# Kernel tuning notes

Measured on AMD Instinct MI355X. Metric: run time of the kernel, lower is better.

## Reference

```python
import jax, jax.numpy as jnp
import numpy as np

CHUNK = 128  # single steady-state chunk tier (T divisible by 128)
DECAY_MIN = 0.005


def setup_inputs() -> dict:
    key = jax.random.key(0)
    k0, k1, k2, k3, k4 = jax.random.split(key, 5)
    B, H, T, K = 4, 16, 2048, 64
    r = jax.random.normal(k0, (B, H, T, K), jnp.float32) * 0.5
    k = jax.random.normal(k1, (B, H, T, K), jnp.float32) * 0.5
    v = jax.random.normal(k2, (B, H, T, K), jnp.float32)
    # log-space decay (negative); mild magnitude keeps exp() of cumulative
    # in-chunk decays within fp32 range (torch original upcasts to fp64)
    w = -(jax.random.uniform(k3, (B, H, T, K), jnp.float32) * 0.2 + 0.01)
    u = jax.random.normal(k4, (1, H, 1, K), jnp.float32) * 0.5
    wkv_state = jnp.zeros((B, H, K, K), jnp.float32)
    return {"r": r, "k": k, "v": v, "w": w, "u": u, "wkv_state": wkv_state}


def _chunked_wkv(r, k, v, w, u, wkv_state):
    B, H, T, K = r.shape
    Tc = CHUNK
    N = T // Tc
    # decay preprocessing (log space)
    w_decay = jnp.clip(jnp.exp(w), DECAY_MIN, None)
    w_log = jnp.log(w_decay)
    wc = w_log.reshape(B, H, N, Tc, K)
    wc_cum = jnp.cumsum(wc, axis=-2)                       # inclusive cumsum
    shifted = jnp.pad(wc_cum[..., :-1, :], ((0, 0), (0, 0), (0, 0), (1, 0), (0, 0)))
    ws = wc.sum(axis=-2, keepdims=True)                    # (B,H,N,1,K)
    w_inter = jnp.exp(ws - wc_cum)                          # (B,H,N,Tc,K)
    w_intra = jnp.exp(wc_cum - wc)
    ws_e = jnp.exp(jnp.swapaxes(ws, -1, -2))               # (B,H,N,K,1)

    rc = r.reshape(B, H, N, Tc, K)
    kc = k.reshape(B, H, N, Tc, K)
    vc = v.reshape(B, H, N, Tc, K)

    # numerically-centered intra-chunk decays (offset at chunk midpoint)
    off = shifted[..., Tc // 2:Tc // 2 + 1, :]
    r_dec = jnp.exp(shifted - off)
    k_inv = jnp.exp(off - wc_cum)

    # intra-chunk attention: strictly-lower-triangular + u-bonus diagonal
    a = jnp.einsum('bhnik,bhnjk->bhnij', rc * r_dec, kc * k_inv)
    a = jnp.tril(a, -1)
    diag = jnp.einsum('bhntk,bhntk->bhnt', rc, u[:, :, None] * kc)
    a = a + diag[..., :, None] * jnp.eye(Tc, dtype=a.dtype)
    out = jnp.einsum('bhnij,bhnjv->bhniv', a, vc)

    # inter-chunk: sequential state carry via scan
    wkv = jnp.einsum('bhntk,bhntv->bhnkv', kc * w_inter, vc)   # (B,H,N,K,K)

    def step(state, inp):
        ws_i, wkv_i = inp
        return state * ws_i + wkv_i, state

    ws_s = jnp.moveaxis(ws_e, 2, 0)    # (N,B,H,K,1)
    wkv_s = jnp.moveaxis(wkv, 2, 0)    # (N,B,H,K,K)
    final_state, states = jax.lax.scan(step, wkv_state, (ws_s, wkv_s))
    states = jnp.moveaxis(states, 0, 2)  # (B,H,N,K,K) — state entering chunk n

    out = out + jnp.einsum('bhntk,bhnkv->bhntv', rc * w_intra, states)
    return out.reshape(B, H, T, K), final_state


def reference(r, k, v, w, u, wkv_state):
    return _chunked_wkv(r, k, v, w, u, wkv_state)
```

## Files before the change

kernel.cpp:

```cpp
#include <hip/hip_runtime.h>

#define TC 128
#define KD 64
#define WLOG_MIN (-5.2983174f)

typedef __attribute__((ext_vector_type(8))) short short8;
typedef __attribute__((ext_vector_type(4))) short short4_t;
typedef __attribute__((ext_vector_type(4))) float f32x4;

__device__ __forceinline__ unsigned short f2bf(float x) {
  union { float f; unsigned int u; } c; c.f = x;
  unsigned int u = c.u + 0x7fffu + ((c.u >> 16) & 1u);
  return (unsigned short)(u >> 16);
}
__device__ __forceinline__ float bf2f(unsigned short x) {
  union { unsigned int u; float f; } c; c.u = ((unsigned int)x) << 16; return c.f;
}


__global__ __launch_bounds__(512, 4)
void rwkv_intra_mfma(const float* __restrict__ rr, const float* __restrict__ kk_,
                     const float* __restrict__ vv, const float* __restrict__ ww,
                     const float* __restrict__ uu, float* __restrict__ out,
                     unsigned short* __restrict__ wkv_u16, float* __restrict__ wse_ws,
                     unsigned short* __restrict__ rw_u16, unsigned short* __restrict__ diag_u16,
                     int H, int N) {
  __shared__ alignas(16) unsigned short rd_s[TC * KD];
  __shared__ alignas(16) unsigned short ki_s[TC * KD];
  __shared__ alignas(16) unsigned short vT_s[KD * TC];
  __shared__ alignas(16) unsigned char su_raw[10240];
  float* segtot = (float*)su_raw;
  unsigned short* Ast = (unsigned short*)su_raw;

  const int bid = blockIdx.x;
  const int n = bid % N, bh = bid / N, h = bh % H;
  const size_t base = ((size_t)bh * N + n) * (TC * KD);
  const float *rg = rr + base, *kg = kk_ + base, *vg = vv + base, *wg = ww + base;
  unsigned short* diagg = diag_u16 + (size_t)bid * TC;

  const int tid = threadIdx.x;
  const int lk = tid & 63;
  const int wv = tid >> 6;

  float wl[16];
  {
    float c = 0.f;
    #pragma unroll
    for (int tt = 0; tt < 16; ++tt) {
      wl[tt] = fmaxf(wg[(wv * 16 + tt) * KD + lk], WLOG_MIN);
      c += wl[tt];
    }
    segtot[wv * 64 + lk] = c;
  }
  __syncthreads();
  float segofs = 0.f, myoff = 0.f, wsum = 0.f;
  #pragma unroll
  for (int i = 0; i < 8; ++i) {
    const float si = segtot[i * 64 + lk];
    if (i < wv) segofs += si;
    if (i < 4) myoff += si;
    wsum += si;
  }
  const float wsoff_own = __expf(wsum - myoff);
  if (wv == 0) wse_ws[((size_t)bh * N + n) * KD + lk] = __expf(wsum);
  const float eoff = __expf(myoff);

  {
    float c = segofs;
    const float uk = uu[h * KD + lk];
    unsigned short* rwg = rw_u16 + base;
    short8 vb8;
    float darr[8];
    #pragma unroll
    for (int tt = 0; tt < 16; ++tt) {
      const int t = wv * 16 + tt;
      float rv = rg[t * KD + lk], kv = kg[t * KD + lk], vvv = vg[t * KD + lk];
      const int slot = (lk >> 3) ^ (t & 7) ^ ((t >> 3) & 7);
      const int nat = t * KD + (slot << 3) + (lk & 7);
      float e1 = __expf(c - myoff);
      rd_s[nat] = f2bf(rv * e1);
      rwg[t * KD + lk] = f2bf(rv * e1 * eoff);
      ki_s[nat] = f2bf(kv * __expf(myoff - c - wl[tt]));
      vb8[tt & 7] = (short)f2bf(vvv);
      darr[tt & 7] = rv * uk * kv;
      c += wl[tt];
      if ((tt & 7) == 7) {
        const int g = t >> 3;
        *(short8*)&vT_s[lk * TC + ((g ^ (lk & 7)) << 3)] = vb8;
        #pragma unroll
        for (int o = 32; o > 0; o >>= 1)
          #pragma unroll
          for (int q = 0; q < 8; ++q) darr[q] += __shfl_xor(darr[q], o, 64);
        if (lk == 0) {
          short8 dpk;
          #pragma unroll
          for (int q = 0; q < 8; ++q) dpk[q] = (short)f2bf(darr[q]);
          *(short8*)&diagg[g * 8] = dpk;
        }
      }
    }
  }
  __syncthreads();

  const int lane = tid & 63, quad = lane >> 4, l16 = lane & 15;

  {
    const int kt = wv >> 1;
    const int nb = (wv & 1) * 2;
    f32x4 acc[2] = {{0,0,0,0},{0,0,0,0}};
    const int kdg = kt * 2 + (l16 >> 3), kd7 = l16 & 7;
    #pragma unroll
    for (int ks = 0; ks < 4; ++ks) {
      short8 a;
      #pragma unroll
      for (int j = 0; j < 8; ++j) {
        const int t = ks * 32 + quad * 8 + j;
        a[j] = (short)ki_s[t * KD + (((kdg ^ (t & 7) ^ ((t >> 3) & 7)) << 3) + kd7)];
      }
      #pragma unroll
      for (int nn = 0; nn < 2; ++nn) {
        const int vd = (nb + nn) * 16 + l16;
        short8 b = *(const short8*)&vT_s[vd * TC + (((ks * 4 + quad) ^ (vd & 7)) << 3)];
        acc[nn] = __builtin_amdgcn_mfma_f32_16x16x32_bf16(a, b, acc[nn], 0, 0, 0);
      }
    }
    float wso[4];
    #pragma unroll
    for (int reg = 0; reg < 4; ++reg) wso[reg] = __shfl(wsoff_own, kt * 16 + quad * 4 + reg, 64);
    unsigned short* wkvg = wkv_u16 + ((size_t)bh * N + n) * (KD * KD);
    #pragma unroll
    for (int nn = 0; nn < 2; ++nn)
      #pragma unroll
      for (int reg = 0; reg < 4; ++reg)
        wkvg[(kt * 16 + quad * 4 + reg) * KD + (nb + nn) * 16 + l16] = f2bf(acc[nn][reg] * wso[reg]);
  }

  {
    const int ib = wv;
    const int i0 = ib * 16;
    const int irow = i0 + l16;
    const int rsw = (irow & 7) ^ ((irow >> 3) & 7);
    short8 b0 = *(const short8*)&rd_s[irow * KD + ((quad ^ rsw) << 3)];
    short8 b1 = *(const short8*)&rd_s[irow * KD + (((4 + quad) ^ rsw) << 3)];
    const float diag_i = bf2f(diagg[irow]);
    f32x4 oacc[4] = {{0,0,0,0},{0,0,0,0},{0,0,0,0},{0,0,0,0}};
    const int npairs = (ib + 2) >> 1;
    unsigned short* astw = Ast + wv * 640;
    for (int jp = 0; jp < npairs; ++jp) {
      #pragma unroll
      for (int jj = 0; jj < 2; ++jj) {
        const int j = jp * 2 + jj;
        short4_t pk;
        if (j <= ib) {
          const int jrow = j * 16 + l16;
          const int jsw = (jrow & 7) ^ ((jrow >> 3) & 7);
          short8 a0 = *(const short8*)&ki_s[jrow * KD + ((quad ^ jsw) << 3)];
          short8 a1 = *(const short8*)&ki_s[jrow * KD + (((4 + quad) ^ jsw) << 3)];
          f32x4 at = {0, 0, 0, 0};
          at = __builtin_amdgcn_mfma_f32_16x16x32_bf16(a0, b0, at, 0, 0, 0);
          at = __builtin_amdgcn_mfma_f32_16x16x32_bf16(a1, b1, at, 0, 0, 0);
          #pragma unroll
          for (int reg = 0; reg < 4; ++reg) {
            const int je = j * 16 + quad * 4 + reg;
            float val = at[reg];
            if (j == ib) val = (je < irow) ? val : ((je == irow) ? diag_i : 0.f);
            pk[reg] = (short)f2bf(val);
          }
        } else {
          pk = (short4_t)0;
        }
        *(short4_t*)&astw[l16 * 40 + jj * 16 + quad * 4] = pk;
      }
      short8 af = *(const short8*)&astw[l16 * 40 + quad * 8];
      #pragma unroll
      for (int nn = 0; nn < 4; ++nn) {
        const int vd = nn * 16 + l16;
        short8 bv = *(const short8*)&vT_s[vd * TC + (((jp * 4 + quad) ^ (vd & 7)) << 3)];
        oacc[nn] = __builtin_amdgcn_mfma_f32_16x16x32_bf16(af, bv, oacc[nn], 0, 0, 0);
      }
    }
    float* og = out + base;
    #pragma unroll
    for (int nn = 0; nn < 4; ++nn)
      #pragma unroll
      for (int reg = 0; reg < 4; ++reg)
        og[(i0 + quad * 4 + reg) * KD + nn * 16 + l16] = oacc[nn][reg];
  }
}

__global__ __launch_bounds__(256, 6)
void rwkv_scan_apply(const unsigned short* __restrict__ wkv_u16,
                     const float* __restrict__ wse_ws,
                     const float* __restrict__ st_in,
                     const unsigned short* __restrict__ rw_u16,
                     float* __restrict__ out, float* __restrict__ final_out, int N) {
  __shared__ alignas(16) unsigned short sT[KD * KD];
  __shared__ alignas(16) float obuf[64 * 68];

  const int bid = blockIdx.x;
  const int n = bid % N, bh = bid / N;
  const int tid = threadIdx.x;

  const int kd = tid >> 2, v0 = (tid & 3) * 16;
  const size_t sbase = (size_t)bh * (KD * KD);
  float s[16];
  #pragma unroll
  for (int i = 0; i < 16; i += 4)
    *(f32x4*)&s[i] = *(const f32x4*)&st_in[sbase + kd * KD + v0 + i];

  const float* wseb = wse_ws + (size_t)bh * N * KD + kd;
  const unsigned short* wkvb = wkv_u16 + (size_t)bh * N * (KD * KD) + kd * KD + v0;

  {
    float e_c = 0.f; short8 x0_c = {0}, x1_c = {0};
    if (n > 0) {
      e_c = wseb[0];
      x0_c = *(const short8*)&wkvb[0];
      x1_c = *(const short8*)&wkvb[8];
    }
    for (int j = 0; j < n; ++j) {
      const float e = e_c; const short8 x0 = x0_c, x1 = x1_c;
      if (j + 1 < n) {
        e_c = wseb[(size_t)(j + 1) * KD];
        x0_c = *(const short8*)&wkvb[(size_t)(j + 1) * (KD * KD)];
        x1_c = *(const short8*)&wkvb[(size_t)(j + 1) * (KD * KD) + 8];
      }
      #pragma unroll
      for (int i = 0; i < 8; ++i) {
        s[i]     = s[i]     * e + bf2f((unsigned short)x0[i]);
        s[i + 8] = s[i + 8] * e + bf2f((unsigned short)x1[i]);
      }
    }
  }

  {
    const int g = kd >> 3, k7 = kd & 7;
    #pragma unroll
    for (int i = 0; i < 16; ++i) {
      const int vd = v0 + i;
      sT[vd * KD + (((g ^ (vd & 7)) << 3) | k7)] = f2bf(s[i]);
    }
  }

  if (n == N - 1) {
    const float e = wseb[(size_t)(N - 1) * KD];
    const short8 x0 = *(const short8*)&wkvb[(size_t)(N - 1) * (KD * KD)];
    const short8 x1 = *(const short8*)&wkvb[(size_t)(N - 1) * (KD * KD) + 8];
    #pragma unroll
    for (int i = 0; i < 8; ++i) {
      s[i]     = s[i]     * e + bf2f((unsigned short)x0[i]);
      s[i + 8] = s[i + 8] * e + bf2f((unsigned short)x1[i]);
    }
    #pragma unroll
    for (int i = 0; i < 16; i += 4)
      *(f32x4*)&final_out[sbase + kd * KD + v0 + i] = *(const f32x4*)&s[i];
  }
  __syncthreads();

  const int lane = tid & 63, wv = tid >> 6, quad = lane >> 4, l16 = lane & 15;
  const unsigned short* rwg = rw_u16 + ((size_t)bh * N + n) * (TC * KD);
  float* og = out + ((size_t)bh * N + n) * (TC * KD);
  #pragma unroll
  for (int half = 0; half < 2; ++half) {
    const int mt = wv + half * 4;
    const int trow = mt * 16 + l16;
    short8 a0 = *(const short8*)&rwg[trow * KD + quad * 8];
    short8 a1 = *(const short8*)&rwg[trow * KD + 32 + quad * 8];
    const int lr0 = (mt - half * 4) * 16 + quad * 4;
    #pragma unroll
    for (int nn = 0; nn < 4; ++nn) {
      const int vd = nn * 16 + l16;
      short8 b0 = *(const short8*)&sT[vd * KD + ((quad ^ (vd & 7)) << 3)];
      short8 b1 = *(const short8*)&sT[vd * KD + (((4 + quad) ^ (vd & 7)) << 3)];
      f32x4 acc = {0, 0, 0, 0};
      acc = __builtin_amdgcn_mfma_f32_16x16x32_bf16(a0, b0, acc, 0, 0, 0);
      acc = __builtin_amdgcn_mfma_f32_16x16x32_bf16(a1, b1, acc, 0, 0, 0);
      #pragma unroll
      for (int reg = 0; reg < 4; ++reg)
        obuf[(lr0 + reg) * 68 + nn * 16 + l16] = acc[reg];
    }
    __syncthreads();
    {
      float* ogh = og + half * 64 * KD;
      #pragma unroll
      for (int i = 0; i < 4; ++i) {
        const int f = tid + i * 256;
        const int row = f >> 4, c4 = (f & 15) * 4;
        f32x4 l = *(const f32x4*)&obuf[row * 68 + c4];
        f32x4 gv = *(const f32x4*)&ogh[row * KD + c4];
        gv += l;
        *(f32x4*)&ogh[row * KD + c4] = gv;
      }
    }
    __syncthreads();
  }
}

extern "C" void kernel_launch(void* const* d_in, const int* in_sizes, int n_in,
                              void* d_out, int out_size, void* d_ws, size_t ws_size,
                              hipStream_t stream) {
  const float* r = (const float*)d_in[0];
  const float* k = (const float*)d_in[1];
  const float* v = (const float*)d_in[2];
  const float* w = (const float*)d_in[3];
  const float* u = (const float*)d_in[4];
  const float* st0 = (const float*)d_in[5];
  float* out = (float*)d_out;

  const int BH = in_sizes[5] / (KD * KD);
  const int H = in_sizes[4] / KD;
  const int T = in_sizes[0] / (BH * KD);
  const int N = T / TC;

  unsigned short* wkv_u16 = (unsigned short*)d_ws;
  float* wse_ws = (float*)(wkv_u16 + (size_t)BH * N * KD * KD);
  unsigned short* rw_u16 = (unsigned short*)(wse_ws + (size_t)BH * N * KD);
  unsigned short* diag_u16 = rw_u16 + (size_t)BH * T * KD;
  float* final_out = out + (size_t)in_sizes[0];

  rwkv_intra_mfma<<<BH * N, 512, 0, stream>>>(r, k, v, w, u, out, wkv_u16, wse_ws,
                                              rw_u16, diag_u16, H, N);
  rwkv_scan_apply<<<BH * N, 256, 0, stream>>>(wkv_u16, wse_ws, st0, rw_u16,
                                              out, final_out, N);
}
```

Before: 198.3 us.

## Split wkv chunk summary into light kernel and fuse intra-chunk with scan-apply

Restructures the two-kernel pipeline. The first kernel now only computes the per-chunk k·v state contributions and decay totals. The second kernel recomputes the intra-chunk attention, runs the prefix scan over earlier chunks, and adds the inter-chunk term in registers before a single write of the output. This removes the bf16 rw and diag intermediates and the read-modify-write of the output in global memory. In exchange, k, v and w are read twice and each block of the heavier kernel performs the sequential scan itself.

```diff
diff --git a/kernel.cpp b/kernel.cpp
--- a/kernel.cpp
+++ b/kernel.cpp
@@ -18,25 +18,19 @@
 }
 
 
-__global__ __launch_bounds__(512, 4)
-void rwkv_intra_mfma(const float* __restrict__ rr, const float* __restrict__ kk_,
-                     const float* __restrict__ vv, const float* __restrict__ ww,
-                     const float* __restrict__ uu, float* __restrict__ out,
-                     unsigned short* __restrict__ wkv_u16, float* __restrict__ wse_ws,
-                     unsigned short* __restrict__ rw_u16, unsigned short* __restrict__ diag_u16,
-                     int H, int N) {
-  __shared__ alignas(16) unsigned short rd_s[TC * KD];
-  __shared__ alignas(16) unsigned short ki_s[TC * KD];
+__global__ __launch_bounds__(512, 8)
+void rwkv_wkv(const float* __restrict__ kk_, const float* __restrict__ vv,
+              const float* __restrict__ ww,
+              unsigned short* __restrict__ wkv_u16, float* __restrict__ wse_ws,
+              int N) {
   __shared__ alignas(16) unsigned short vT_s[KD * TC];
-  __shared__ alignas(16) unsigned char su_raw[10240];
-  float* segtot = (float*)su_raw;
-  unsigned short* Ast = (unsigned short*)su_raw;
+  __shared__ alignas(16) unsigned short kiT_s[KD * TC];
+  __shared__ alignas(16) float segtot[8 * 64];
 
   const int bid = blockIdx.x;
-  const int n = bid % N, bh = bid / N, h = bh % H;
+  const int n = bid % N, bh = bid / N;
   const size_t base = ((size_t)bh * N + n) * (TC * KD);
-  const float *rg = rr + base, *kg = kk_ + base, *vg = vv + base, *wg = ww + base;
-  unsigned short* diagg = diag_u16 + (size_t)bid * TC;
+  const float *kg = kk_ + base, *vg = vv + base, *wg = ww + base;
 
   const int tid = threadIdx.x;
   const int lk = tid & 63;
@@ -63,23 +57,118 @@
   }
   const float wsoff_own = __expf(wsum - myoff);
   if (wv == 0) wse_ws[((size_t)bh * N + n) * KD + lk] = __expf(wsum);
+
+  {
+    float c = segofs;
+    short8 vb8, kib8;
+    #pragma unroll
+    for (int tt = 0; tt < 16; ++tt) {
+      const int t = wv * 16 + tt;
+      const float kv = kg[t * KD + lk], vvv = vg[t * KD + lk];
+      kib8[tt & 7] = (short)f2bf(kv * __expf(myoff - c - wl[tt]));
+      vb8[tt & 7] = (short)f2bf(vvv);
+      c += wl[tt];
+      if ((tt & 7) == 7) {
+        const int g = t >> 3;
+        *(short8*)&vT_s[lk * TC + ((g ^ (lk & 7)) << 3)] = vb8;
+        *(short8*)&kiT_s[lk * TC + ((g ^ (lk & 7)) << 3)] = kib8;
+      }
+    }
+  }
+  __syncthreads();
+
+  {
+    const int quad = lk >> 4, l16 = lk & 15;
+    const int kt = wv >> 1;
+    const int nb = (wv & 1) * 2;
+    f32x4 acc[2] = {{0,0,0,0},{0,0,0,0}};
+    const int row = kt * 16 + l16;
+    #pragma unroll
+    for (int ks = 0; ks < 4; ++ks) {
+      short8 a = *(const short8*)&kiT_s[row * TC + (((ks * 4 + quad) ^ (row & 7)) << 3)];
+      #pragma unroll
+      for (int nn = 0; nn < 2; ++nn) {
+        const int vd = (nb + nn) * 16 + l16;
+        short8 b = *(const short8*)&vT_s[vd * TC + (((ks * 4 + quad) ^ (vd & 7)) << 3)];
+        acc[nn] = __builtin_amdgcn_mfma_f32_16x16x32_bf16(a, b, acc[nn], 0, 0, 0);
+      }
+    }
+    float wso[4];
+    #pragma unroll
+    for (int reg = 0; reg < 4; ++reg) wso[reg] = __shfl(wsoff_own, kt * 16 + quad * 4 + reg, 64);
+    unsigned short* wkvg = wkv_u16 + ((size_t)bh * N + n) * (KD * KD);
+    #pragma unroll
+    for (int nn = 0; nn < 2; ++nn)
+      #pragma unroll
+      for (int reg = 0; reg < 4; ++reg)
+        wkvg[(kt * 16 + quad * 4 + reg) * KD + (nb + nn) * 16 + l16] = f2bf(acc[nn][reg] * wso[reg]);
+  }
+}
+
+__global__ __launch_bounds__(512, 4)
+void rwkv_main(const float* __restrict__ rr, const float* __restrict__ kk_,
+               const float* __restrict__ vv, const float* __restrict__ ww,
+               const float* __restrict__ uu,
+               const unsigned short* __restrict__ wkv_u16,
+               const float* __restrict__ wse_ws,
+               const float* __restrict__ st_in,
+               float* __restrict__ out, float* __restrict__ final_out,
+               int H, int N) {
+  __shared__ alignas(16) unsigned short rd_s[TC * KD];
+  __shared__ alignas(16) unsigned short ki_s[TC * KD];
+  __shared__ alignas(16) unsigned short vT_s[KD * TC];
+  __shared__ alignas(16) unsigned char su_raw[10240];
+  __shared__ alignas(16) unsigned short diag_s[TC];
+  float* segtot = (float*)su_raw;
+  unsigned short* Ast = (unsigned short*)su_raw;
+
+  const int bid = blockIdx.x;
+  const int n = bid % N, bh = bid / N, h = bh % H;
+  const size_t base = ((size_t)bh * N + n) * (TC * KD);
+  const float *rg = rr + base, *kg = kk_ + base, *vg = vv + base, *wg = ww + base;
+
+  const int tid = threadIdx.x;
+  const int lk = tid & 63;
+  const int wv = tid >> 6;
+  const int quad = lk >> 4, l16 = lk & 15;
+  const float uk = uu[h * KD + lk];
+
+  float wl[16];
+  {
+    float c = 0.f;
+    #pragma unroll
+    for (int tt = 0; tt < 16; ++tt) {
+      wl[tt] = fmaxf(wg[(wv * 16 + tt) * KD + lk], WLOG_MIN);
+      c += wl[tt];
+    }
+    segtot[wv * 64 + lk] = c;
+  }
+  __syncthreads();
+  float segofs = 0.f, myoff = 0.f;
+  #pragma unroll
+  for (int i = 0; i < 8; ++i) {
+    const float si = segtot[i * 64 + lk];
+    if (i < wv) segofs += si;
+    if (i < 4) myoff += si;
+  }
   const float eoff = __expf(myoff);
 
+  unsigned int rwp[8];
   {
     float c = segofs;
-    const float uk = uu[h * KD + lk];
-    unsigned short* rwg = rw_u16 + base;
     short8 vb8;
     float darr[8];
     #pragma unroll
     for (int tt = 0; tt < 16; ++tt) {
       const int t = wv * 16 + tt;
-      float rv = rg[t * KD + lk], kv = kg[t * KD + lk], vvv = vg[t * KD + lk];
+      const float rv = rg[t * KD + lk], kv = kg[t * KD + lk], vvv = vg[t * KD + lk];
       const int slot = (lk >> 3) ^ (t & 7) ^ ((t >> 3) & 7);
       const int nat = t * KD + (slot << 3) + (lk & 7);
-      float e1 = __expf(c - myoff);
+      const float e1 = __expf(c - myoff);
       rd_s[nat] = f2bf(rv * e1);
-      rwg[t * KD + lk] = f2bf(rv * e1 * eoff);
+      const unsigned short rwv = f2bf(rv * e1 * eoff);
+      if (tt & 1) rwp[tt >> 1] |= ((unsigned int)rwv) << 16;
+      else        rwp[tt >> 1]  = (unsigned int)rwv;
       ki_s[nat] = f2bf(kv * __expf(myoff - c - wl[tt]));
       vb8[tt & 7] = (short)f2bf(vvv);
       darr[tt & 7] = rv * uk * kv;
@@ -95,55 +184,46 @@
           short8 dpk;
           #pragma unroll
           for (int q = 0; q < 8; ++q) dpk[q] = (short)f2bf(darr[q]);
-          *(short8*)&diagg[g * 8] = dpk;
+          *(short8*)&diag_s[g * 8] = dpk;
         }
       }
     }
   }
   __syncthreads();
 
-  const int lane = tid & 63, quad = lane >> 4, l16 = lane & 15;
-
-  {
-    const int kt = wv >> 1;
-    const int nb = (wv & 1) * 2;
-    f32x4 acc[2] = {{0,0,0,0},{0,0,0,0}};
-    const int kdg = kt * 2 + (l16 >> 3), kd7 = l16 & 7;
-    #pragma unroll
-    for (int ks = 0; ks < 4; ++ks) {
-      short8 a;
-      #pragma unroll
-      for (int j = 0; j < 8; ++j) {
-        const int t = ks * 32 + quad * 8 + j;
-        a[j] = (short)ki_s[t * KD + (((kdg ^ (t & 7) ^ ((t >> 3) & 7)) << 3) + kd7)];
-      }
-      #pragma unroll
-      for (int nn = 0; nn < 2; ++nn) {
-        const int vd = (nb + nn) * 16 + l16;
-        short8 b = *(const short8*)&vT_s[vd * TC + (((ks * 4 + quad) ^ (vd & 7)) << 3)];
-        acc[nn] = __builtin_amdgcn_mfma_f32_16x16x32_bf16(a, b, acc[nn], 0, 0, 0);
-      }
-    }
-    float wso[4];
-    #pragma unroll
-    for (int reg = 0; reg < 4; ++reg) wso[reg] = __shfl(wsoff_own, kt * 16 + quad * 4 + reg, 64);
-    unsigned short* wkvg = wkv_u16 + ((size_t)bh * N + n) * (KD * KD);
-    #pragma unroll
-    for (int nn = 0; nn < 2; ++nn)
-      #pragma unroll
-      for (int reg = 0; reg < 4; ++reg)
-        wkvg[(kt * 16 + quad * 4 + reg) * KD + (nb + nn) * 16 + l16] = f2bf(acc[nn][reg] * wso[reg]);
-  }
-
-  {
-    const int ib = wv;
-    const int i0 = ib * 16;
-    const int irow = i0 + l16;
+  const int skd = tid >> 3, sv0 = (tid & 7) * 8;
+  const size_t sbase = (size_t)bh * (KD * KD);
+  float s[8];
+  *(f32x4*)&s[0] = *(const f32x4*)&st_in[sbase + skd * KD + sv0];
+  *(f32x4*)&s[4] = *(const f32x4*)&st_in[sbase + skd * KD + sv0 + 4];
+  const float* wseb = wse_ws + (size_t)bh * N * KD + skd;
+  const unsigned short* wkvb = wkv_u16 + (size_t)bh * N * (KD * KD) + skd * KD + sv0;
+  {
+    float e_c = 0.f; short8 x_c = {0};
+    if (n > 0) {
+      e_c = wseb[0];
+      x_c = *(const short8*)&wkvb[0];
+    }
+    for (int j = 0; j < n; ++j) {
+      const float e = e_c; const short8 x = x_c;
+      if (j + 1 < n) {
+        e_c = wseb[(size_t)(j + 1) * KD];
+        x_c = *(const short8*)&wkvb[(size_t)(j + 1) * (KD * KD)];
+      }
+      #pragma unroll
+      for (int i = 0; i < 8; ++i) s[i] = s[i] * e + bf2f((unsigned short)x[i]);
+    }
+  }
+
+  f32x4 oacc[4];
+  {
+    const int ib = wv, i0 = ib * 16, irow = i0 + l16;
     const int rsw = (irow & 7) ^ ((irow >> 3) & 7);
     short8 b0 = *(const short8*)&rd_s[irow * KD + ((quad ^ rsw) << 3)];
     short8 b1 = *(const short8*)&rd_s[irow * KD + (((4 + quad) ^ rsw) << 3)];
-    const float diag_i = bf2f(diagg[irow]);
-    f32x4 oacc[4] = {{0,0,0,0},{0,0,0,0},{0,0,0,0},{0,0,0,0}};
+    const float diag_i = bf2f(diag_s[irow]);
+    #pragma unroll
+    for (int nn = 0; nn < 4; ++nn) oacc[nn] = (f32x4){0, 0, 0, 0};
     const int npairs = (ib + 2) >> 1;
     unsigned short* astw = Ast + wv * 640;
     for (int jp = 0; jp < npairs; ++jp) {
@@ -179,120 +259,53 @@
         oacc[nn] = __builtin_amdgcn_mfma_f32_16x16x32_bf16(af, bv, oacc[nn], 0, 0, 0);
       }
     }
+  }
+  __syncthreads();
+
+  {
+    const int g = skd >> 3, k7 = skd & 7;
+    #pragma unroll
+    for (int i = 0; i < 8; ++i) {
+      const int vd = sv0 + i;
+      ki_s[vd * KD + (((g ^ (vd & 7)) << 3) | k7)] = f2bf(s[i]);
+    }
+  }
+  #pragma unroll
+  for (int tt = 0; tt < 16; ++tt) {
+    const int t = wv * 16 + tt;
+    const int slot = (lk >> 3) ^ (t & 7) ^ ((t >> 3) & 7);
+    const int nat = t * KD + (slot << 3) + (lk & 7);
+    const unsigned int pa = rwp[tt >> 1];
+    rd_s[nat] = (unsigned short)((tt & 1) ? (pa >> 16) : (pa & 0xffffu));
+  }
+  if (n == N - 1) {
+    const float e = wseb[(size_t)n * KD];
+    const short8 x = *(const short8*)&wkvb[(size_t)n * (KD * KD)];
+    #pragma unroll
+    for (int i = 0; i < 8; ++i) s[i] = s[i] * e + bf2f((unsigned short)x[i]);
+    *(f32x4*)&final_out[sbase + skd * KD + sv0] = *(const f32x4*)&s[0];
+    *(f32x4*)&final_out[sbase + skd * KD + sv0 + 4] = *(const f32x4*)&s[4];
+  }
+  __syncthreads();
+
+  {
+    const int ib = wv, trow = ib * 16 + l16;
+    const int rsw = (trow & 7) ^ ((trow >> 3) & 7);
+    short8 a0 = *(const short8*)&rd_s[trow * KD + ((quad ^ rsw) << 3)];
+    short8 a1 = *(const short8*)&rd_s[trow * KD + (((4 + quad) ^ rsw) << 3)];
     float* og = out + base;
-    #pragma unroll
-    for (int nn = 0; nn < 4; ++nn)
-      #pragma unroll
-      for (int reg = 0; reg < 4; ++reg)
-        og[(i0 + quad * 4 + reg) * KD + nn * 16 + l16] = oacc[nn][reg];
-  }
-}
-
-__global__ __launch_bounds__(256, 6)
-void rwkv_scan_apply(const unsigned short* __restrict__ wkv_u16,
-                     const float* __restrict__ wse_ws,
-                     const float* __restrict__ st_in,
-                     const unsigned short* __restrict__ rw_u16,
-                     float* __restrict__ out, float* __restrict__ final_out, int N) {
-  __shared__ alignas(16) unsigned short sT[KD * KD];
-  __shared__ alignas(16) float obuf[64 * 68];
-
-  const int bid = blockIdx.x;
-  const int n = bid % N, bh = bid / N;
-  const int tid = threadIdx.x;
-
-  const int kd = tid >> 2, v0 = (tid & 3) * 16;
-  const size_t sbase = (size_t)bh * (KD * KD);
-  float s[16];
-  #pragma unroll
-  for (int i = 0; i < 16; i += 4)
-    *(f32x4*)&s[i] = *(const f32x4*)&st_in[sbase + kd * KD + v0 + i];
-
-  const float* wseb = wse_ws + (size_t)bh * N * KD + kd;
-  const unsigned short* wkvb = wkv_u16 + (size_t)bh * N * (KD * KD) + kd * KD + v0;
-
-  {
-    float e_c = 0.f; short8 x0_c = {0}, x1_c = {0};
-    if (n > 0) {
-      e_c = wseb[0];
-      x0_c = *(const short8*)&wkvb[0];
-      x1_c = *(const short8*)&wkvb[8];
-    }
-    for (int j = 0; j < n; ++j) {
-      const float e = e_c; const short8 x0 = x0_c, x1 = x1_c;
-      if (j + 1 < n) {
-        e_c = wseb[(size_t)(j + 1) * KD];
-        x0_c = *(const short8*)&wkvb[(size_t)(j + 1) * (KD * KD)];
-        x1_c = *(const short8*)&wkvb[(size_t)(j + 1) * (KD * KD) + 8];
-      }
-      #pragma unroll
-      for (int i = 0; i < 8; ++i) {
-        s[i]     = s[i]     * e + bf2f((unsigned short)x0[i]);
-        s[i + 8] = s[i + 8] * e + bf2f((unsigned short)x1[i]);
-      }
-    }
-  }
-
-  {
-    const int g = kd >> 3, k7 = kd & 7;
-    #pragma unroll
-    for (int i = 0; i < 16; ++i) {
-      const int vd = v0 + i;
-      sT[vd * KD + (((g ^ (vd & 7)) << 3) | k7)] = f2bf(s[i]);
-    }
-  }
-
-  if (n == N - 1) {
-    const float e = wseb[(size_t)(N - 1) * KD];
-    const short8 x0 = *(const short8*)&wkvb[(size_t)(N - 1) * (KD * KD)];
-    const short8 x1 = *(const short8*)&wkvb[(size_t)(N - 1) * (KD * KD) + 8];
-    #pragma unroll
-    for (int i = 0; i < 8; ++i) {
-      s[i]     = s[i]     * e + bf2f((unsigned short)x0[i]);
-      s[i + 8] = s[i + 8] * e + bf2f((unsigned short)x1[i]);
-    }
-    #pragma unroll
-    for (int i = 0; i < 16; i += 4)
-      *(f32x4*)&final_out[sbase + kd * KD + v0 + i] = *(const f32x4*)&s[i];
-  }
-  __syncthreads();
-
-  const int lane = tid & 63, wv = tid >> 6, quad = lane >> 4, l16 = lane & 15;
-  const unsigned short* rwg = rw_u16 + ((size_t)bh * N + n) * (TC * KD);
-  float* og = out + ((size_t)bh * N + n) * (TC * KD);
-  #pragma unroll
-  for (int half = 0; half < 2; ++half) {
-    const int mt = wv + half * 4;
-    const int trow = mt * 16 + l16;
-    short8 a0 = *(const short8*)&rwg[trow * KD + quad * 8];
-    short8 a1 = *(const short8*)&rwg[trow * KD + 32 + quad * 8];
-    const int lr0 = (mt - half * 4) * 16 + quad * 4;
     #pragma unroll
     for (int nn = 0; nn < 4; ++nn) {
       const int vd = nn * 16 + l16;
-      short8 b0 = *(const short8*)&sT[vd * KD + ((quad ^ (vd & 7)) << 3)];
-      short8 b1 = *(const short8*)&sT[vd * KD + (((4 + quad) ^ (vd & 7)) << 3)];
+      short8 b0 = *(const short8*)&ki_s[vd * KD + ((quad ^ (vd & 7)) << 3)];
+      short8 b1 = *(const short8*)&ki_s[vd * KD + (((4 + quad) ^ (vd & 7)) << 3)];
       f32x4 acc = {0, 0, 0, 0};
       acc = __builtin_amdgcn_mfma_f32_16x16x32_bf16(a0, b0, acc, 0, 0, 0);
       acc = __builtin_amdgcn_mfma_f32_16x16x32_bf16(a1, b1, acc, 0, 0, 0);
       #pragma unroll
       for (int reg = 0; reg < 4; ++reg)
-        obuf[(lr0 + reg) * 68 + nn * 16 + l16] = acc[reg];
-    }
-    __syncthreads();
-    {
-      float* ogh = og + half * 64 * KD;
-      #pragma unroll
-      for (int i = 0; i < 4; ++i) {
-        const int f = tid + i * 256;
-        const int row = f >> 4, c4 = (f & 15) * 4;
-        f32x4 l = *(const f32x4*)&obuf[row * 68 + c4];
-        f32x4 gv = *(const f32x4*)&ogh[row * KD + c4];
-        gv += l;
-        *(f32x4*)&ogh[row * KD + c4] = gv;
-      }
-    }
-    __syncthreads();
+        og[(size_t)(ib * 16 + quad * 4 + reg) * KD + nn * 16 + l16] = oacc[nn][reg] + acc[reg];
+    }
   }
 }
 
@@ -314,12 +327,9 @@
 
   unsigned short* wkv_u16 = (unsigned short*)d_ws;
   float* wse_ws = (float*)(wkv_u16 + (size_t)BH * N * KD * KD);
-  unsigned short* rw_u16 = (unsigned short*)(wse_ws + (size_t)BH * N * KD);
-  unsigned short* diag_u16 = rw_u16 + (size_t)BH * T * KD;
   float* final_out = out + (size_t)in_sizes[0];
 
-  rwkv_intra_mfma<<<BH * N, 512, 0, stream>>>(r, k, v, w, u, out, wkv_u16, wse_ws,
-                                              rw_u16, diag_u16, H, N);
-  rwkv_scan_apply<<<BH * N, 256, 0, stream>>>(wkv_u16, wse_ws, st0, rw_u16,
-                                              out, final_out, N);
-}
+  rwkv_wkv<<<BH * N, 512, 0, stream>>>(k, v, w, wkv_u16, wse_ws, N);
+  rwkv_main<<<BH * N, 512, 0, stream>>>(r, k, v, w, u, wkv_u16, wse_ws, st0,
+                                        out, final_out, H, N);
+}
```

Measured after the change: 194.8 us. About the same (-1.7%).
